# Kernel optimization log

Measured on AMD Instinct MI355X. Metric: run time of the kernel, lower is better.

Reference implementation:

```python
import jax, jax.numpy as jnp
import numpy as np

EMBED = 1024
HEADS = 16

def setup_inputs() -> dict:
    key = jax.random.key(0)
    k1, k2, k3, k4, k5 = jax.random.split(key, 5)
    x = jax.random.normal(k1, (2, 2048, EMBED), dtype=jnp.float32)
    s = 1.0 / np.sqrt(EMBED)
    W_atten = jax.random.normal(k2, (EMBED, 3 * EMBED), dtype=jnp.float32) * s
    b_atten = jax.random.normal(k3, (3 * EMBED,), dtype=jnp.float32) * 0.01
    W_proj = jax.random.normal(k4, (EMBED, EMBED), dtype=jnp.float32) * s
    b_proj = jax.random.normal(k5, (EMBED,), dtype=jnp.float32) * 0.01
    return {"x": x, "W_atten": W_atten, "b_atten": b_atten, "W_proj": W_proj, "b_proj": b_proj}

def reference(x, W_atten, b_atten, W_proj, b_proj):
    B, T, C = x.shape
    H = HEADS
    hs = C // H
    qkv = x @ W_atten + b_atten  # [B,T,3C]
    # NOTE: original splits as k, q, v (k first)
    k, q, v = jnp.split(qkv, 3, axis=2)
    k = k.reshape(B, T, H, hs).transpose(0, 2, 1, 3)  # [B,H,T,hs]
    q = q.reshape(B, T, H, hs).transpose(0, 2, 1, 3)
    v = v.reshape(B, T, H, hs).transpose(0, 2, 1, 3)
    scores = jnp.einsum('bhqd,bhkd->bhqk', q, k) / jnp.sqrt(jnp.float32(hs))
    causal = jnp.tril(jnp.ones((T, T), dtype=bool))
    scores = jnp.where(causal[None, None, :, :], scores, jnp.float32(-jnp.inf))
    att = jax.nn.softmax(scores, axis=-1)
    out = jnp.einsum('bhqk,bhkd->bhqd', att, v)  # [B,H,T,hs]
    out = out.transpose(0, 2, 1, 3).reshape(B, T, C)
    return out @ W_proj + b_proj
```

## Files before the change

### kernel.cpp

```cpp
#include <hip/hip_runtime.h>

typedef unsigned short u16;
typedef unsigned int u32;
typedef __bf16 bf16;
typedef bf16 bf16x8 __attribute__((ext_vector_type(8)));
typedef float f32x4 __attribute__((ext_vector_type(4)));
typedef u32 u32x4 __attribute__((ext_vector_type(4)));
typedef u16 u16x4 __attribute__((ext_vector_type(4)));

#define EMBED 1024
#define HEADS 16
#define HS 64
#define BATCH 2
#define SEQ 2048
#define M_TOT (BATCH * SEQ)
#define N_QKV (3 * EMBED)
#define KDIM  EMBED

#define CSCALE 0.18033688011112042f
#define MREF (64.0f * CSCALE)

__device__ __forceinline__ u16 f2bf(float f) {
  u32 u = __builtin_bit_cast(u32, f);
  u32 r = u + 0x7fffu + ((u >> 16) & 1u);
  return (u16)(r >> 16);
}
__device__ __forceinline__ float bf2f(u16 h) {
  return __builtin_bit_cast(float, (u32)h << 16);
}
__device__ __forceinline__ bf16x8 frag16(const u16* p) {
  return __builtin_bit_cast(bf16x8, *(const u32x4*)p);
}
__device__ __forceinline__ bf16x8 frag16u(const u32* p) {
  return __builtin_bit_cast(bf16x8, *(const u32x4*)p);
}
__device__ __forceinline__ float cl(float v) {
  return fminf(fmaxf(v, -3.0e4f), 3.0e4f);
}
__device__ __forceinline__ u32 pk2bf(float lo, float hi) {
  const u32 ul = __builtin_bit_cast(u32, lo) + 0x8000u;
  const u32 uh = __builtin_bit_cast(u32, hi) + 0x8000u;
  return (ul >> 16) | (uh & 0xFFFF0000u);
}

typedef __attribute__((address_space(1))) void gvoid;
typedef __attribute__((address_space(3))) void lvoid;
__device__ __forceinline__ void glds16(const u16* g, u16* l) {
  __builtin_amdgcn_global_load_lds((gvoid*)g, (lvoid*)l, 16, 0, 0);
}

__global__ __launch_bounds__(256) void convert_kernel(
    const float* __restrict__ in, u16* __restrict__ out, int n4) {
  const int i = blockIdx.x * 256 + threadIdx.x;
  if (i < n4) {
    f32x4 v = *(const f32x4*)(in + (size_t)i * 4);
    u16x4 pk;
#pragma unroll
    for (int j = 0; j < 4; j++) pk[j] = f2bf(v[j]);
    *(u16x4*)(out + (size_t)i * 4) = pk;
  }
}

__global__ __launch_bounds__(256) void transpose_conv_kernel(
    const float* __restrict__ in, u16* __restrict__ out, int R, int C) {
  __shared__ u16 tile[32][33];
  const int c0 = blockIdx.x * 32;
  const int r0 = blockIdx.y * 32;
  const int tx = threadIdx.x;
  const int ty = threadIdx.y;
#pragma unroll
  for (int i = 0; i < 32; i += 8)
    tile[ty + i][tx] = f2bf(in[(size_t)(r0 + ty + i) * C + c0 + tx]);
  __syncthreads();
#pragma unroll
  for (int i = 0; i < 32; i += 8)
    out[(size_t)(c0 + ty + i) * R + r0 + tx] = tile[tx][ty + i];
}

__global__ __launch_bounds__(256) void gemm_qkv_kernel(
    const u16* __restrict__ A, const u16* __restrict__ wt,
    const u16* __restrict__ bias, u16* __restrict__ kq, u16* __restrict__ vt) {
  __shared__ u16 As[128 * 32];
  __shared__ u16 Bs[128 * 32];
  const int tid = threadIdx.x;
  const int lane = tid & 63;
  const int wave = tid >> 6;
  const int quad = lane >> 4;
  const int l16 = lane & 15;
  const int wr = wave >> 1;
  const int wc = wave & 1;
  const int m0 = blockIdx.y * 128;
  const int n0 = blockIdx.x * 128;

  f32x4 acc[4][4] = {};
  const int grow = tid >> 2;
  const int gcol = (tid & 3) * 8;

  for (int k0 = 0; k0 < KDIM; k0 += 32) {
    __syncthreads();
    glds16(A + (size_t)(m0 + grow) * KDIM + k0 + gcol, As + tid * 8);
    glds16(A + (size_t)(m0 + grow + 64) * KDIM + k0 + gcol, As + 2048 + tid * 8);
    glds16(wt + (size_t)(n0 + grow) * KDIM + k0 + gcol, Bs + tid * 8);
    glds16(wt + (size_t)(n0 + grow + 64) * KDIM + k0 + gcol, Bs + 2048 + tid * 8);
    __syncthreads();

    bf16x8 af[4], bfr[4];
#pragma unroll
    for (int i = 0; i < 4; i++) {
      af[i]  = frag16(As + (wr * 64 + i * 16 + l16) * 32 + quad * 8);
      bfr[i] = frag16(Bs + (wc * 64 + i * 16 + l16) * 32 + quad * 8);
    }
#pragma unroll
    for (int mi = 0; mi < 4; mi++)
#pragma unroll
      for (int ni = 0; ni < 4; ni++)
        acc[mi][ni] = __builtin_amdgcn_mfma_f32_16x16x32_bf16(
            af[mi], bfr[ni], acc[mi][ni], 0, 0, 0);
  }

#pragma unroll
  for (int ni = 0; ni < 4; ni++) {
    const int n = n0 + wc * 64 + ni * 16 + l16;
    const float bv = bf2f(bias[n]);
    if (n < 2 * EMBED) {
#pragma unroll
      for (int mi = 0; mi < 4; mi++)
#pragma unroll
        for (int r = 0; r < 4; r++) {
          const int m = m0 + wr * 64 + mi * 16 + quad * 4 + r;
          kq[(size_t)m * 2048 + n] = f2bf(cl(acc[mi][ni][r] + bv));
        }
    } else {
      const int hd = n - 2 * EMBED;
      const int h2 = hd >> 6;
      const int dc2 = (hd >> 4) & 3;
#pragma unroll
      for (int mi = 0; mi < 4; mi++) {
        const int mbase = m0 + wr * 64 + mi * 16 + quad * 4;
        const int bqi = mbase >> 11;
        const int t0 = mbase & 2047;
        const int kt2 = t0 >> 6;
        const int kc2 = (t0 >> 5) & 1;
        const int qt2 = (t0 >> 3) & 3;
        const int e0 = t0 & 7;
        u16x4 pk;
#pragma unroll
        for (int r = 0; r < 4; r++) pk[r] = f2bf(cl(acc[mi][ni][r] + bv));
        const size_t idx =
            ((((size_t)(bqi * 16 + h2) * 32 + kt2) * 2 + kc2) * 4 + dc2) * 512 +
            (qt2 * 16 + l16) * 8 + e0;
        *(u16x4*)(vt + idx) = pk;
      }
    }
  }
}

__global__ __launch_bounds__(128) void gemm_proj_kernel(
    const u16* __restrict__ A, const u16* __restrict__ wt,
    const u16* __restrict__ bias, float* __restrict__ out) {
  __shared__ u16 As[128 * 32];
  __shared__ u16 Bs[64 * 32];
  const int tid = threadIdx.x;
  const int lane = tid & 63;
  const int wave = tid >> 6;
  const int quad = lane >> 4;
  const int l16 = lane & 15;
  const int m0 = blockIdx.y * 128;
  const int n0 = blockIdx.x * 64;

  f32x4 acc[4][4] = {};
  const int grow = tid >> 2;
  const int gcol = (tid & 3) * 8;

  for (int k0 = 0; k0 < KDIM; k0 += 32) {
    __syncthreads();
#pragma unroll
    for (int p = 0; p < 4; p++)
      glds16(A + (size_t)(m0 + p * 32 + grow) * KDIM + k0 + gcol,
             As + p * 1024 + tid * 8);
#pragma unroll
    for (int p = 0; p < 2; p++)
      glds16(wt + (size_t)(n0 + p * 32 + grow) * KDIM + k0 + gcol,
             Bs + p * 1024 + tid * 8);
    __syncthreads();

    bf16x8 af[4], bfr[4];
#pragma unroll
    for (int i = 0; i < 4; i++) {
      af[i]  = frag16(As + (wave * 64 + i * 16 + l16) * 32 + quad * 8);
      bfr[i] = frag16(Bs + (i * 16 + l16) * 32 + quad * 8);
    }
#pragma unroll
    for (int mi = 0; mi < 4; mi++)
#pragma unroll
      for (int ni = 0; ni < 4; ni++)
        acc[mi][ni] = __builtin_amdgcn_mfma_f32_16x16x32_bf16(
            af[mi], bfr[ni], acc[mi][ni], 0, 0, 0);
  }

#pragma unroll
  for (int ni = 0; ni < 4; ni++) {
    const int n = n0 + ni * 16 + l16;
    const float bv = bf2f(bias[n]);
#pragma unroll
    for (int mi = 0; mi < 4; mi++)
#pragma unroll
      for (int r = 0; r < 4; r++) {
        const int m = m0 + wave * 64 + mi * 16 + quad * 4 + r;
        out[(size_t)m * EMBED + n] = cl(acc[mi][ni][r] + bv);
      }
  }
}

__global__ __launch_bounds__(128) void attn_kernel(
    const u16* __restrict__ kq, const u16* __restrict__ vt,
    u16* __restrict__ att) {
  __shared__ u16 Ks[2][2][64 * 64];
  __shared__ u32 Ps32[2][2][16 * 32];

  const int tid = threadIdx.x;
  const int lane = tid & 63;
  const int wave = tid >> 6;
  const int quad = (lane >> 4) & 3;
  const int l16 = lane & 15;

  const int bh = blockIdx.x;
  const int yy = (int)blockIdx.y;
  const int qt32 = wave ? yy : (63 - yy);
  const int q0 = qt32 * 32;
  const int bq = bh >> 4;
  const int h = bh & 15;

  int qg[2];
  bf16x8 bq0[2], bq1[2];
#pragma unroll
  for (int g = 0; g < 2; g++) {
    qg[g] = q0 + g * 16 + l16;
    const size_t qrow = (size_t)(bq * SEQ + qg[g]) * 2048 + EMBED + h * HS;
    bq0[g] = frag16(kq + qrow + quad * 8);
    bq1[g] = frag16(kq + qrow + 32 + quad * 8);
  }

  const u16* kb = kq + (size_t)bq * SEQ * 2048 + h * HS;
  const u16* vb2 = vt + (size_t)(bq * 16 + h) * 32 * 4096;
  const int psw32 = (l16 & 7) << 2;
  const int sw = quad ^ (l16 & 7);

  u32x4 onesu;
#pragma unroll
  for (int j = 0; j < 4; j++) onesu[j] = 0x3F803F80u;
  const bf16x8 ones8 = __builtin_bit_cast(bf16x8, onesu);

  f32x4 o[2][4] = {};
  f32x4 o4[2] = {};

  const int nkt = (qt32 >> 1) + 1;
  u16* ksw = (u16*)Ks[wave];

#pragma unroll
  for (int p = 0; p < 8; p++) {
    const int row = p * 8 + (lane >> 3);
    const int sgc = (lane & 7) ^ (row & 7);
    glds16(kb + (size_t)row * 2048 + sgc * 8, ksw + row * 64 + (lane & 7) * 8);
  }

  for (int kt = 0; kt < nkt; kt++) {
    const int k0 = kt * 64;
    asm volatile("s_waitcnt vmcnt(0)" ::: "memory");
    if (kt + 1 < nkt) {
      const int kn = k0 + 64;
      u16* dst = ksw + ((kt + 1) & 1) * (64 * 64);
#pragma unroll
      for (int p = 0; p < 8; p++) {
        const int row = p * 8 + (lane >> 3);
        const int sgc = (lane & 7) ^ (row & 7);
        glds16(kb + (size_t)(kn + row) * 2048 + sgc * 8, dst + row * 64 + (lane & 7) * 8);
      }
    }
    const u16* KsB = ksw + (kt & 1) * (64 * 64);

    bf16x8 va[2][4];
#pragma unroll
    for (int kc = 0; kc < 2; kc++)
#pragma unroll
      for (int dc = 0; dc < 4; dc++)
        va[kc][dc] = frag16(vb2 + (size_t)kt * 4096 +
                            ((kc * 4 + dc) * 64 + quad * 16 + l16) * 8);

    f32x4 st[2][4] = {};
    __builtin_amdgcn_s_setprio(1);
#pragma unroll
    for (int sub = 0; sub < 4; sub++) {
      const u16* kr = KsB + (sub * 16 + l16) * 64;
      const bf16x8 ka0 = frag16(kr + sw * 8);
      const bf16x8 ka1 = frag16(kr + (sw ^ 4) * 8);
#pragma unroll
      for (int g = 0; g < 2; g++) {
        st[g][sub] = __builtin_amdgcn_mfma_f32_16x16x32_bf16(
            ka0, bq0[g], st[g][sub], 0, 0, 0);
        st[g][sub] = __builtin_amdgcn_mfma_f32_16x16x32_bf16(
            ka1, bq1[g], st[g][sub], 0, 0, 0);
      }
    }
    __builtin_amdgcn_s_setprio(0);

    const bool diag = (kt == nkt - 1);
#pragma unroll
    for (int g = 0; g < 2; g++) {
      float p[4][4];
      if (diag) {
#pragma unroll
        for (int sub = 0; sub < 4; sub++)
#pragma unroll
          for (int r = 0; r < 4; r++) {
            const int key = k0 + sub * 16 + quad * 4 + r;
            const float e = __builtin_amdgcn_exp2f(st[g][sub][r] * CSCALE - MREF);
            p[sub][r] = (key <= qg[g]) ? e : 0.0f;
          }
      } else {
#pragma unroll
        for (int sub = 0; sub < 4; sub++)
#pragma unroll
          for (int r = 0; r < 4; r++)
            p[sub][r] = __builtin_amdgcn_exp2f(st[g][sub][r] * CSCALE - MREF);
      }
      u32* pw = Ps32[wave][g];
#pragma unroll
      for (int sub = 0; sub < 4; sub++)
#pragma unroll
        for (int rp = 0; rp < 2; rp++)
          pw[l16 * 32 + ((sub * 8 + quad * 2 + rp) ^ psw32)] =
              pk2bf(p[sub][2 * rp], p[sub][2 * rp + 1]);
    }

#pragma unroll
    for (int g = 0; g < 2; g++) {
      u32* pw = Ps32[wave][g];
#pragma unroll
      for (int kc = 0; kc < 2; kc++) {
        bf16x8 pb = frag16u(pw + l16 * 32 + ((kc * 16 + quad * 4) ^ psw32));
        __builtin_amdgcn_s_setprio(1);
#pragma unroll
        for (int dc = 0; dc < 4; dc++)
          o[g][dc] = __builtin_amdgcn_mfma_f32_16x16x32_bf16(
              va[kc][dc], pb, o[g][dc], 0, 0, 0);
        o4[g] = __builtin_amdgcn_mfma_f32_16x16x32_bf16(
            ones8, pb, o4[g], 0, 0, 0);
        __builtin_amdgcn_s_setprio(0);
      }
    }
  }

#pragma unroll
  for (int g = 0; g < 2; g++) {
    const float inv = 1.0f / o4[g][0];
    const size_t obase = (size_t)(bq * SEQ + qg[g]) * EMBED + h * HS;
#pragma unroll
    for (int dc = 0; dc < 4; dc++) {
      u16 sv[4];
#pragma unroll
      for (int r = 0; r < 4; r++) sv[r] = f2bf(cl(o[g][dc][r] * inv));
      *(u32*)(att + obase + dc * 16 + quad * 4) = (u32)sv[0] | ((u32)sv[1] << 16);
      *(u32*)(att + obase + dc * 16 + quad * 4 + 2) = (u32)sv[2] | ((u32)sv[3] << 16);
    }
  }
}

extern "C" void kernel_launch(void* const* d_in, const int* in_sizes, int n_in,
                              void* d_out, int out_size, void* d_ws,
                              size_t ws_size, hipStream_t stream) {
  const float* x       = (const float*)d_in[0];
  const float* W_atten = (const float*)d_in[1];
  const float* b_atten = (const float*)d_in[2];
  const float* W_proj  = (const float*)d_in[3];
  const float* b_proj  = (const float*)d_in[4];

  u16* wt_a = (u16*)d_ws;
  u16* wt_p = wt_a + (size_t)N_QKV * EMBED;
  u16* ba   = wt_p + (size_t)EMBED * EMBED;
  u16* bp   = ba + N_QKV;
  u16* xb   = bp + EMBED;
  u16* kq   = xb + (size_t)M_TOT * KDIM;
  u16* vt   = kq + (size_t)M_TOT * 2048;
  u16* attb = xb;

  convert_kernel<<<(M_TOT * KDIM / 4 + 255) / 256, 256, 0, stream>>>(
      x, xb, M_TOT * KDIM / 4);
  convert_kernel<<<(N_QKV / 4 + 255) / 256, 256, 0, stream>>>(b_atten, ba, N_QKV / 4);
  convert_kernel<<<(EMBED / 4 + 255) / 256, 256, 0, stream>>>(b_proj, bp, EMBED / 4);
  transpose_conv_kernel<<<dim3(N_QKV / 32, EMBED / 32), dim3(32, 8), 0, stream>>>(
      W_atten, wt_a, EMBED, N_QKV);
  transpose_conv_kernel<<<dim3(EMBED / 32, EMBED / 32), dim3(32, 8), 0, stream>>>(
      W_proj, wt_p, EMBED, EMBED);
  gemm_qkv_kernel<<<dim3(N_QKV / 128, M_TOT / 128), 256, 0, stream>>>(
      xb, wt_a, ba, kq, vt);
  attn_kernel<<<dim3(BATCH * HEADS, SEQ / 64), 128, 0, stream>>>(kq, vt, attb);
  gemm_proj_kernel<<<dim3(EMBED / 64, M_TOT / 128), 128, 0, stream>>>(
      attb, wt_p, bp, (float*)d_out);
}
```

Baseline: 196.4 us.

## Replace LDS round-trip of P with cross-lane shuffles via permuted key rows

Permutes which K rows each lane loads so the S accumulator layout lines up with the B-operand layout needed for the PV MFMA. The probability tile is then assembled in registers with two xor-32 shuffles per chunk instead of being written to shared memory and read back. This removes the P shared buffer and its LDS write/read traffic. In exchange it adds lane-select logic and DPP/permute shuffles, and it depends on the permutation mapping being exactly right.

```diff
diff --git a/kernel.cpp b/kernel.cpp
--- a/kernel.cpp
+++ b/kernel.cpp
@@ -216,13 +216,13 @@
     const u16* __restrict__ kq, const u16* __restrict__ vt,
     u16* __restrict__ att) {
   __shared__ u16 Ks[2][2][64 * 64];
-  __shared__ u32 Ps32[2][2][16 * 32];
 
   const int tid = threadIdx.x;
   const int lane = tid & 63;
   const int wave = tid >> 6;
   const int quad = (lane >> 4) & 3;
   const int l16 = lane & 15;
+  const bool lohalf = (lane < 32);
 
   const int bh = blockIdx.x;
   const int yy = (int)blockIdx.y;
@@ -243,8 +243,11 @@
 
   const u16* kb = kq + (size_t)bq * SEQ * 2048 + h * HS;
   const u16* vb2 = vt + (size_t)(bq * 16 + h) * 32 * 4096;
-  const int psw32 = (l16 & 7) << 2;
-  const int sw = quad ^ (l16 & 7);
+
+  const int pi = ((l16 >> 2) & 1) * 8 + ((l16 >> 3) & 1) * 2 +
+                 ((l16 >> 1) & 1) * 4 + (l16 & 1);
+  const int psw = quad ^ (pi & 7);
+  const int kap = (quad & 1) * 8 + ((quad >> 1) & 1) * 2;
 
   u32x4 onesu;
 #pragma unroll
@@ -291,9 +294,9 @@
     __builtin_amdgcn_s_setprio(1);
 #pragma unroll
     for (int sub = 0; sub < 4; sub++) {
-      const u16* kr = KsB + (sub * 16 + l16) * 64;
-      const bf16x8 ka0 = frag16(kr + sw * 8);
-      const bf16x8 ka1 = frag16(kr + (sw ^ 4) * 8);
+      const u16* kr = KsB + (sub * 16 + pi) * 64;
+      const bf16x8 ka0 = frag16(kr + psw * 8);
+      const bf16x8 ka1 = frag16(kr + (psw ^ 4) * 8);
 #pragma unroll
       for (int g = 0; g < 2; g++) {
         st[g][sub] = __builtin_amdgcn_mfma_f32_16x16x32_bf16(
@@ -313,7 +316,7 @@
         for (int sub = 0; sub < 4; sub++)
 #pragma unroll
           for (int r = 0; r < 4; r++) {
-            const int key = k0 + sub * 16 + quad * 4 + r;
+            const int key = k0 + sub * 16 + kap + (r >> 1) * 4 + (r & 1);
             const float e = __builtin_amdgcn_exp2f(st[g][sub][r] * CSCALE - MREF);
             p[sub][r] = (key <= qg[g]) ? e : 0.0f;
           }
@@ -324,21 +327,23 @@
           for (int r = 0; r < 4; r++)
             p[sub][r] = __builtin_amdgcn_exp2f(st[g][sub][r] * CSCALE - MREF);
       }
-      u32* pw = Ps32[wave][g];
-#pragma unroll
-      for (int sub = 0; sub < 4; sub++)
-#pragma unroll
-        for (int rp = 0; rp < 2; rp++)
-          pw[l16 * 32 + ((sub * 8 + quad * 2 + rp) ^ psw32)] =
-              pk2bf(p[sub][2 * rp], p[sub][2 * rp + 1]);
-    }
-
-#pragma unroll
-    for (int g = 0; g < 2; g++) {
-      u32* pw = Ps32[wave][g];
+
 #pragma unroll
       for (int kc = 0; kc < 2; kc++) {
-        bf16x8 pb = frag16u(pw + l16 * 32 + ((kc * 16 + quad * 4) ^ psw32));
+        const int s0 = kc * 2, s1 = kc * 2 + 1;
+        const u32 An = pk2bf(p[s0][0], p[s0][1]);
+        const u32 Bn = pk2bf(p[s1][0], p[s1][1]);
+        const u32 Cn = pk2bf(p[s0][2], p[s0][3]);
+        const u32 Dn = pk2bf(p[s1][2], p[s1][3]);
+        const u32 V1 = __shfl_xor(lohalf ? Bn : An, 32);
+        const u32 V2 = __shfl_xor(lohalf ? Dn : Cn, 32);
+        u32x4 pr;
+        pr[0] = lohalf ? An : V1;
+        pr[1] = lohalf ? V1 : Bn;
+        pr[2] = lohalf ? Cn : V2;
+        pr[3] = lohalf ? V2 : Dn;
+        const bf16x8 pb = __builtin_bit_cast(bf16x8, pr);
+
         __builtin_amdgcn_s_setprio(1);
 #pragma unroll
         for (int dc = 0; dc < 4; dc++)
```

Result: no change. 193.3 us (-1.6%).
